# Optimization experiments

Measured on AMD Instinct MI355X. Metric: run time of the kernel, lower is better.

The kernel has to match this reference:

```python
import jax, jax.numpy as jnp
import numpy as np

F_FACETS = 400000
TEX_PER = 4            # textures per facet (counts sum must equal total textures)
T_TEX = F_FACETS * TEX_PER
C_IN = 64
C_OUT = 64
L = 2
N_BASIS = (L + 1) ** 2  # 9
BN_EPS = 1e-3


def setup_inputs() -> dict:
    key = jax.random.key(0)
    k1, k2, k3 = jax.random.split(key, 3)
    input_texture = jax.random.normal(k1, (T_TEX, C_IN), jnp.float32)
    bary_coeff = jax.random.uniform(k2, (T_TEX, N_BASIS), jnp.float32)
    # per-facet texture counts; constant 4 so counts sum exactly to T_TEX
    num_texture = jnp.full((F_FACETS,), TEX_PER, dtype=jnp.int32)
    # xavier_normal_ on [O, I, K]: fan_in = I*K, fan_out = ... torch uses fan_in=I*K? For 3D it treats dim1*rest.
    std = float(np.sqrt(2.0 / (C_IN * N_BASIS + C_OUT * N_BASIS)))
    weights = jax.random.normal(k3, (C_OUT, C_IN, N_BASIS), jnp.float32) * std
    biases = jnp.zeros((1, C_OUT), jnp.float32)
    gamma = jnp.ones((C_OUT,), jnp.float32)
    beta = jnp.zeros((C_OUT,), jnp.float32)
    return {
        "input_texture": input_texture,
        "bary_coeff": bary_coeff,
        "weights": weights,
        "biases": biases,
        "gamma": gamma,
        "beta": beta,
        "num_texture": num_texture,
    }


def reference(input_texture, bary_coeff, weights, biases, gamma, beta, num_texture):
    T = input_texture.shape[0]
    n_facets = num_texture.shape[0]
    n_basis = weights.shape[2]
    # per-texture contribution: contrib[t,o] = sum_{i,k} x[t,i] * W[o,i,k] * bary[t,k]
    # loop over small fixed basis count (9) to avoid a [T, I, K] intermediate
    contrib = jnp.zeros((T, weights.shape[0]), dtype=input_texture.dtype)
    for k in range(n_basis):
        contrib = contrib + (input_texture @ weights[:, :, k].T) * bary_coeff[:, k:k + 1]
    # scatter-sum per facet (ragged groups given by num_texture), then average
    seg_ids = jnp.repeat(jnp.arange(n_facets), num_texture, total_repeat_length=T)
    facet_sum = jax.ops.segment_sum(contrib, seg_ids, num_segments=n_facets)
    out = facet_sum / num_texture[:, None].astype(facet_sum.dtype)
    # bias + ReLU
    out = jax.nn.relu(out + biases)
    # BatchNorm1d in training mode: batch stats (biased variance), eps=1e-3
    mu = jnp.mean(out, axis=0)
    var = jnp.mean(jnp.square(out - mu), axis=0)
    out = (out - mu) * jax.lax.rsqrt(var + BN_EPS) * gamma + beta
    return out
```

## Files before the change

kernel.cpp:

```cpp
#include <hip/hip_runtime.h>


typedef _Float16 half8  __attribute__((ext_vector_type(8)));
typedef _Float16 h2     __attribute__((ext_vector_type(2)));
typedef __fp16   fp16x2 __attribute__((ext_vector_type(2)));
typedef float    f32x4  __attribute__((ext_vector_type(4)));

#define NGROUPS 100000
#define FFACETS 400000
#define GRID1   768
#define LDSBUF  8192

#define WAITV(N) asm volatile("s_waitcnt vmcnt(" #N ")" ::: "memory")
#define FENCE()  asm volatile("" ::: "memory")

union HF { h2 h[4]; half8 v; };

static __device__ __forceinline__ h2 pkrtz(float a, float b) {
    fp16x2 r = __builtin_amdgcn_cvt_pkrtz(a, b);
    return __builtin_bit_cast(h2, r);
}

static __device__ __forceinline__ void gload16(const void* g, void* l) {
    __builtin_amdgcn_global_load_lds((const __attribute__((address_space(1))) void*)g,
                                     (__attribute__((address_space(3))) void*)l, 16, 0, 0);
}

__global__ __launch_bounds__(256) void prep_kernel(const float* __restrict__ W,
                                                   _Float16* __restrict__ wswz,
                                                   float* __restrict__ stats) {
    int idx = blockIdx.x * 256 + threadIdx.x;
    if (idx < 36864) {
        int j    = idx & 7;
        int lane = (idx >> 3) & 63;
        int mt   = (idx >> 9) & 3;
        int c    = idx >> 11;
        int o    = mt * 16 + (lane & 15);
        int i    = (c & 1) * 32 + ((lane >> 4) << 3) + j;
        int kb   = c >> 1;
        wswz[idx] = (_Float16)W[(o * 64 + i) * 9 + kb];
    }
    if (idx < 128) stats[idx] = 0.0f;
}

__global__ __launch_bounds__(256, 3) void pass1_kernel(
    const float* __restrict__ X, const float* __restrict__ BARY,
    const _Float16* __restrict__ WSWZ, const float* __restrict__ BIAS,
    const int* __restrict__ NTEX, float* __restrict__ OUT,
    float* __restrict__ stats) {

    __shared__ __align__(16) char lds[2][LDSBUF];
    __shared__ float sl_s[64];
    __shared__ float sl_s2[64];

    const int tid  = threadIdx.x;
    const int wave = tid >> 6;
    const int lane = tid & 63;
    const int col  = lane & 15;
    const int quad = lane >> 4;

    half8 wf[18];
#pragma unroll
    for (int c = 0; c < 18; ++c)
        wf[c] = *(const half8*)(WSWZ + ((size_t)(c * 4 + wave) * 64 + lane) * 8);

    const f32x4 biasv = *(const f32x4*)(BIAS + wave * 16 + quad * 4);

    const int pphys  = (wave << 10) + (lane << 4);
    const int xsoff  = pphys ^ (((pphys >> 8) & 7) << 4);
    const char* Xb   = (const char*)X;
    const char* BNb  = (lane < 36) ? ((const char*)BARY + lane * 16) : (const char*)NTEX;

    const int m    = (col & 7) << 4;
    const int a00  = (col << 8) + ((quad << 5) ^ m);
    const int a10  = (col << 8) + (((quad << 5) | 16) ^ m);
    const int bco  = 4096 + col * 36;
    const int nco  = 4096 + 576 + ((col >> 2) << 2);

    float sacc[4]  = {0.f, 0.f, 0.f, 0.f};
    float s2acc[4] = {0.f, 0.f, 0.f, 0.f};

    const int b = blockIdx.x;
    const int n = (NGROUPS - 1 - b) / GRID1 + 1;

    auto STAGE = [&](int p, int g) {
        gload16(Xb + (size_t)g * 4096 + xsoff, &lds[p][pphys]);
        if (lane < 37) {
            size_t so = (lane < 36) ? (size_t)g * 576 : (size_t)g * 16;
            gload16(BNb + so, &lds[p][4096 + lane * 16]);
        }
    };

    auto ITER = [&](int p, int g, int gpre, bool do_stage) {
        __builtin_amdgcn_s_barrier();
        FENCE();
        f32x4 r00 = *(const f32x4*)&lds[p][a00];
        f32x4 r10 = *(const f32x4*)&lds[p][a10];
        f32x4 r01 = *(const f32x4*)&lds[p][a00 + 128];
        f32x4 r11 = *(const f32x4*)&lds[p][a10 + 128];
        float bF[9];
#pragma unroll
        for (int k = 0; k < 9; ++k) bF[k] = *(const float*)&lds[p][bco + k * 4];
        const int nt = *(const int*)&lds[p][nco];
        asm volatile("s_waitcnt lgkmcnt(0)" ::: "memory");
        __builtin_amdgcn_sched_barrier(0);
        __builtin_amdgcn_s_barrier();
        FENCE();
        if (do_stage) STAGE(p, gpre);
        FENCE();

        h2 xh[8], bh[9];
        xh[0] = pkrtz(r00[0], r00[1]);  xh[1] = pkrtz(r00[2], r00[3]);
        xh[2] = pkrtz(r10[0], r10[1]);  xh[3] = pkrtz(r10[2], r10[3]);
        xh[4] = pkrtz(r01[0], r01[1]);  xh[5] = pkrtz(r01[2], r01[3]);
        xh[6] = pkrtz(r11[0], r11[1]);  xh[7] = pkrtz(r11[2], r11[3]);
#pragma unroll
        for (int k = 0; k < 9; ++k) bh[k] = pkrtz(bF[k], bF[k]);
        const float rc = __builtin_amdgcn_rcpf((float)nt);

        f32x4 acc0 = {0.f, 0.f, 0.f, 0.f};
        f32x4 acc1 = {0.f, 0.f, 0.f, 0.f};
        __builtin_amdgcn_s_setprio(1);
#pragma unroll
        for (int c = 0; c < 18; c += 2) {
            const h2 bk = bh[c >> 1];
            HF bf0, bf1;
            bf0.h[0] = xh[0] * bk;  bf0.h[1] = xh[1] * bk;
            bf0.h[2] = xh[2] * bk;  bf0.h[3] = xh[3] * bk;
            acc0 = __builtin_amdgcn_mfma_f32_16x16x32_f16(wf[c], bf0.v, acc0, 0, 0, 0);
            bf1.h[0] = xh[4] * bk;  bf1.h[1] = xh[5] * bk;
            bf1.h[2] = xh[6] * bk;  bf1.h[3] = xh[7] * bk;
            acc1 = __builtin_amdgcn_mfma_f32_16x16x32_f16(wf[c + 1], bf1.v, acc1, 0, 0, 0);
        }
        __builtin_amdgcn_s_setprio(0);

        const int f = g * 4 + (col >> 2);
        f32x4 vv;
#pragma unroll
        for (int r = 0; r < 4; ++r) {
            float s = acc0[r] + acc1[r];
            s += __shfl_xor(s, 1);
            s += __shfl_xor(s, 2);
            s = s * rc + biasv[r];
            s = s > 0.f ? s : 0.f;
            vv[r] = s;
            sacc[r]  += s;
            s2acc[r] += s * s;
        }
        if ((col & 3) == 0)
            *(f32x4*)(OUT + (size_t)f * 64 + wave * 16 + quad * 4) = vv;
    };

    STAGE(0, b);
    STAGE(1, b + GRID1);
    WAITV(2); ITER(0, b,         b + 2 * GRID1, true);
    WAITV(3); ITER(1, b + GRID1, b + 3 * GRID1, true);
    int t = 2;
    for (; t < n - 2; ++t) {
        WAITV(4);
        ITER(t & 1, b + t * GRID1, b + (t + 2) * GRID1, true);
    }
    WAITV(4); ITER(t & 1, b + t * GRID1, 0, false); ++t;
    WAITV(0); ITER(t & 1, b + t * GRID1, 0, false);

#pragma unroll
    for (int r = 0; r < 4; ++r) {
        float s = sacc[r], s2 = s2acc[r];
        s  += __shfl_xor(s, 1);  s  += __shfl_xor(s, 2);
        s  += __shfl_xor(s, 4);  s  += __shfl_xor(s, 8);
        s2 += __shfl_xor(s2, 1); s2 += __shfl_xor(s2, 2);
        s2 += __shfl_xor(s2, 4); s2 += __shfl_xor(s2, 8);
        if (col == 0) {
            sl_s [wave * 16 + quad * 4 + r] = s  * 0.25f;
            sl_s2[wave * 16 + quad * 4 + r] = s2 * 0.25f;
        }
    }
    __syncthreads();
    if (tid < 64)        atomicAdd(&stats[tid],      sl_s [tid]);
    else if (tid < 128)  atomicAdd(&stats[tid],      sl_s2[tid - 64]);
}

__global__ __launch_bounds__(256) void pass3_kernel(float* __restrict__ OUT,
    const float* __restrict__ stats, const float* __restrict__ gamma,
    const float* __restrict__ beta) {
    const int tid = threadIdx.x;
    const size_t l = (size_t)blockIdx.x * 256 + tid;
    const int c0 = ((int)l & 15) * 4;
    float mu[4], sc[4], be[4];
    const float invF = 1.0f / (float)FFACETS;
#pragma unroll
    for (int u = 0; u < 4; ++u) {
        int ch = c0 + u;
        float m  = stats[ch] * invF;
        float va = stats[64 + ch] * invF - m * m;
        mu[u] = m;
        sc[u] = rsqrtf(va + 1e-3f) * gamma[ch];
        be[u] = beta[ch];
    }
    const size_t n4 = (size_t)FFACETS * 16;
    for (size_t i = l; i < n4; i += (size_t)gridDim.x * 256) {
        f32x4 v = ((f32x4*)OUT)[i];
#pragma unroll
        for (int u = 0; u < 4; ++u)
            v[u] = (v[u] - mu[u]) * sc[u] + be[u];
        ((f32x4*)OUT)[i] = v;
    }
}

extern "C" void kernel_launch(void* const* d_in, const int* in_sizes, int n_in,
                              void* d_out, int out_size, void* d_ws, size_t ws_size,
                              hipStream_t stream) {
    const float* X     = (const float*)d_in[0];
    const float* BARY  = (const float*)d_in[1];
    const float* W     = (const float*)d_in[2];
    const float* BIAS  = (const float*)d_in[3];
    const float* GAMMA = (const float*)d_in[4];
    const float* BETA  = (const float*)d_in[5];
    const int*   NTEX  = (const int*)d_in[6];
    float* OUT = (float*)d_out;

    _Float16* wswz = (_Float16*)d_ws;
    float* stats   = (float*)((char*)d_ws + 73728);

    prep_kernel<<<144, 256, 0, stream>>>(W, wswz, stats);
    pass1_kernel<<<GRID1, 256, 0, stream>>>(X, BARY, wswz, BIAS, NTEX, OUT, stats);
    pass3_kernel<<<2048, 256, 0, stream>>>(OUT, stats, GAMMA, BETA);
}
```

Measured before the change: 687.9 us.

## Process two facet groups per pipeline iteration with doubled LDS stage

Each pipeline stage now loads two consecutive 16-texture groups (X, barycentric coefficients and counts for 8 facets) into a larger LDS buffer. Each iteration runs two independent 18-MFMA accumulation chains, one per group, instead of splitting one group across two accumulators. The goals are to halve the barrier and stage overhead per group, keep more memory traffic in flight, and give the MFMA units two independent dependency chains to interleave. In exchange the kernel uses more registers and LDS, which may lower occupancy, and the vmcnt wait counts had to be retuned to the new number of loads and stores per stage.

```diff
diff --git a/kernel.cpp b/kernel.cpp
--- a/kernel.cpp
+++ b/kernel.cpp
@@ -7,12 +7,15 @@
 typedef float    f32x4  __attribute__((ext_vector_type(4)));
 
 #define NGROUPS 100000
+#define NPAIRS  50000
 #define FFACETS 400000
 #define GRID1   768
-#define LDSBUF  8192
+#define LDSP    9472
 
 #define WAITV(N) asm volatile("s_waitcnt vmcnt(" #N ")" ::: "memory")
+#define WAITL0() asm volatile("s_waitcnt lgkmcnt(0)" ::: "memory")
 #define FENCE()  asm volatile("" ::: "memory")
+#define SB0()    __builtin_amdgcn_sched_barrier(0)
 
 union HF { h2 h[4]; half8 v; };
 
@@ -49,7 +52,7 @@
     const int* __restrict__ NTEX, float* __restrict__ OUT,
     float* __restrict__ stats) {
 
-    __shared__ __align__(16) char lds[2][LDSBUF];
+    __shared__ __align__(16) char lds[2][LDSP];
     __shared__ float sl_s[64];
     __shared__ float sl_s2[64];
 
@@ -69,76 +72,35 @@
     const int pphys  = (wave << 10) + (lane << 4);
     const int xsoff  = pphys ^ (((pphys >> 8) & 7) << 4);
     const char* Xb   = (const char*)X;
-    const char* BNb  = (lane < 36) ? ((const char*)BARY + lane * 16) : (const char*)NTEX;
+    const char* BAb  = (const char*)BARY;
+    const char* NTb  = (const char*)NTEX;
 
     const int m    = (col & 7) << 4;
     const int a00  = (col << 8) + ((quad << 5) ^ m);
     const int a10  = (col << 8) + (((quad << 5) | 16) ^ m);
-    const int bco  = 4096 + col * 36;
-    const int nco  = 4096 + 576 + ((col >> 2) << 2);
+    const int bco  = 8192 + col * 36;
+    const int nco  = 9344 + ((col >> 2) << 2);
 
     float sacc[4]  = {0.f, 0.f, 0.f, 0.f};
     float s2acc[4] = {0.f, 0.f, 0.f, 0.f};
 
     const int b = blockIdx.x;
-    const int n = (NGROUPS - 1 - b) / GRID1 + 1;
-
-    auto STAGE = [&](int p, int g) {
-        gload16(Xb + (size_t)g * 4096 + xsoff, &lds[p][pphys]);
-        if (lane < 37) {
-            size_t so = (lane < 36) ? (size_t)g * 576 : (size_t)g * 16;
-            gload16(BNb + so, &lds[p][4096 + lane * 16]);
-        }
+    const int n = (NPAIRS - 1 - b) / GRID1 + 1;
+
+    auto STAGE = [&](int p, int u) {
+        const char* xs = Xb + (size_t)u * 8192;
+        gload16(xs + xsoff,        &lds[p][pphys]);
+        gload16(xs + 4096 + xsoff, &lds[p][4096 + pphys]);
+        gload16(BAb + (size_t)u * 1152 + lane * 16, &lds[p][8192 + lane * 16]);
+        if (lane < 8) gload16(BAb + (size_t)u * 1152 + 1024 + lane * 16, &lds[p][9216 + lane * 16]);
+        if (lane < 2) gload16(NTb + (size_t)u * 32 + lane * 16,          &lds[p][9344 + lane * 16]);
     };
 
-    auto ITER = [&](int p, int g, int gpre, bool do_stage) {
-        __builtin_amdgcn_s_barrier();
-        FENCE();
-        f32x4 r00 = *(const f32x4*)&lds[p][a00];
-        f32x4 r10 = *(const f32x4*)&lds[p][a10];
-        f32x4 r01 = *(const f32x4*)&lds[p][a00 + 128];
-        f32x4 r11 = *(const f32x4*)&lds[p][a10 + 128];
-        float bF[9];
-#pragma unroll
-        for (int k = 0; k < 9; ++k) bF[k] = *(const float*)&lds[p][bco + k * 4];
-        const int nt = *(const int*)&lds[p][nco];
-        asm volatile("s_waitcnt lgkmcnt(0)" ::: "memory");
-        __builtin_amdgcn_sched_barrier(0);
-        __builtin_amdgcn_s_barrier();
-        FENCE();
-        if (do_stage) STAGE(p, gpre);
-        FENCE();
-
-        h2 xh[8], bh[9];
-        xh[0] = pkrtz(r00[0], r00[1]);  xh[1] = pkrtz(r00[2], r00[3]);
-        xh[2] = pkrtz(r10[0], r10[1]);  xh[3] = pkrtz(r10[2], r10[3]);
-        xh[4] = pkrtz(r01[0], r01[1]);  xh[5] = pkrtz(r01[2], r01[3]);
-        xh[6] = pkrtz(r11[0], r11[1]);  xh[7] = pkrtz(r11[2], r11[3]);
-#pragma unroll
-        for (int k = 0; k < 9; ++k) bh[k] = pkrtz(bF[k], bF[k]);
-        const float rc = __builtin_amdgcn_rcpf((float)nt);
-
-        f32x4 acc0 = {0.f, 0.f, 0.f, 0.f};
-        f32x4 acc1 = {0.f, 0.f, 0.f, 0.f};
-        __builtin_amdgcn_s_setprio(1);
-#pragma unroll
-        for (int c = 0; c < 18; c += 2) {
-            const h2 bk = bh[c >> 1];
-            HF bf0, bf1;
-            bf0.h[0] = xh[0] * bk;  bf0.h[1] = xh[1] * bk;
-            bf0.h[2] = xh[2] * bk;  bf0.h[3] = xh[3] * bk;
-            acc0 = __builtin_amdgcn_mfma_f32_16x16x32_f16(wf[c], bf0.v, acc0, 0, 0, 0);
-            bf1.h[0] = xh[4] * bk;  bf1.h[1] = xh[5] * bk;
-            bf1.h[2] = xh[6] * bk;  bf1.h[3] = xh[7] * bk;
-            acc1 = __builtin_amdgcn_mfma_f32_16x16x32_f16(wf[c + 1], bf1.v, acc1, 0, 0, 0);
-        }
-        __builtin_amdgcn_s_setprio(0);
-
-        const int f = g * 4 + (col >> 2);
+    auto EPI = [&](f32x4 acc, float rc, int f) {
         f32x4 vv;
 #pragma unroll
         for (int r = 0; r < 4; ++r) {
-            float s = acc0[r] + acc1[r];
+            float s = acc[r];
             s += __shfl_xor(s, 1);
             s += __shfl_xor(s, 2);
             s = s * rc + biasv[r];
@@ -151,17 +113,82 @@
             *(f32x4*)(OUT + (size_t)f * 64 + wave * 16 + quad * 4) = vv;
     };
 
+    auto ITER = [&](int p, int u, int upre, bool do_stage) {
+        __builtin_amdgcn_s_barrier();
+        FENCE();
+        const char* L = lds[p];
+        f32x4 r0[4], r1[4];
+        r0[0] = *(const f32x4*)(L + a00);
+        r0[1] = *(const f32x4*)(L + a10);
+        r0[2] = *(const f32x4*)(L + a00 + 128);
+        r0[3] = *(const f32x4*)(L + a10 + 128);
+        r1[0] = *(const f32x4*)(L + 4096 + a00);
+        r1[1] = *(const f32x4*)(L + 4096 + a10);
+        r1[2] = *(const f32x4*)(L + 4096 + a00 + 128);
+        r1[3] = *(const f32x4*)(L + 4096 + a10 + 128);
+        float bF0[9], bF1[9];
+#pragma unroll
+        for (int k = 0; k < 9; ++k) bF0[k] = *(const float*)(L + bco + k * 4);
+#pragma unroll
+        for (int k = 0; k < 9; ++k) bF1[k] = *(const float*)(L + bco + 576 + k * 4);
+        const int nt0 = *(const int*)(L + nco);
+        const int nt1 = *(const int*)(L + nco + 16);
+
+        h2 xh0[8], xh1[8], bh0[9], bh1[9];
+        xh0[0] = pkrtz(r0[0][0], r0[0][1]);  xh0[1] = pkrtz(r0[0][2], r0[0][3]);
+        xh0[2] = pkrtz(r0[1][0], r0[1][1]);  xh0[3] = pkrtz(r0[1][2], r0[1][3]);
+        xh0[4] = pkrtz(r0[2][0], r0[2][1]);  xh0[5] = pkrtz(r0[2][2], r0[2][3]);
+        xh0[6] = pkrtz(r0[3][0], r0[3][1]);  xh0[7] = pkrtz(r0[3][2], r0[3][3]);
+        xh1[0] = pkrtz(r1[0][0], r1[0][1]);  xh1[1] = pkrtz(r1[0][2], r1[0][3]);
+        xh1[2] = pkrtz(r1[1][0], r1[1][1]);  xh1[3] = pkrtz(r1[1][2], r1[1][3]);
+        xh1[4] = pkrtz(r1[2][0], r1[2][1]);  xh1[5] = pkrtz(r1[2][2], r1[2][3]);
+        xh1[6] = pkrtz(r1[3][0], r1[3][1]);  xh1[7] = pkrtz(r1[3][2], r1[3][3]);
+#pragma unroll
+        for (int k = 0; k < 9; ++k) { bh0[k] = pkrtz(bF0[k], bF0[k]); bh1[k] = pkrtz(bF1[k], bF1[k]); }
+        const float rc0 = __builtin_amdgcn_rcpf((float)nt0);
+        const float rc1 = __builtin_amdgcn_rcpf((float)nt1);
+
+        WAITL0();
+        SB0();
+        __builtin_amdgcn_s_barrier();
+        FENCE();
+        if (do_stage) STAGE(p, upre);
+        FENCE();
+
+        f32x4 accA = {0.f, 0.f, 0.f, 0.f};
+        f32x4 accB = {0.f, 0.f, 0.f, 0.f};
+        __builtin_amdgcn_s_setprio(1);
+#pragma unroll
+        for (int c = 0; c < 18; ++c) {
+            const int hh = (c & 1) * 4;
+            const h2 bkA = bh0[c >> 1];
+            const h2 bkB = bh1[c >> 1];
+            HF fa, fb;
+            fa.h[0] = xh0[hh + 0] * bkA;  fa.h[1] = xh0[hh + 1] * bkA;
+            fa.h[2] = xh0[hh + 2] * bkA;  fa.h[3] = xh0[hh + 3] * bkA;
+            accA = __builtin_amdgcn_mfma_f32_16x16x32_f16(wf[c], fa.v, accA, 0, 0, 0);
+            fb.h[0] = xh1[hh + 0] * bkB;  fb.h[1] = xh1[hh + 1] * bkB;
+            fb.h[2] = xh1[hh + 2] * bkB;  fb.h[3] = xh1[hh + 3] * bkB;
+            accB = __builtin_amdgcn_mfma_f32_16x16x32_f16(wf[c], fb.v, accB, 0, 0, 0);
+        }
+        __builtin_amdgcn_s_setprio(0);
+
+        const int f0 = u * 8 + (col >> 2);
+        EPI(accA, rc0, f0);
+        EPI(accB, rc1, f0 + 4);
+    };
+
     STAGE(0, b);
     STAGE(1, b + GRID1);
-    WAITV(2); ITER(0, b,         b + 2 * GRID1, true);
-    WAITV(3); ITER(1, b + GRID1, b + 3 * GRID1, true);
+    WAITV(5); ITER(0, b,         b + 2 * GRID1, true);
+    WAITV(7); ITER(1, b + GRID1, b + 3 * GRID1, true);
     int t = 2;
     for (; t < n - 2; ++t) {
-        WAITV(4);
+        WAITV(9);
         ITER(t & 1, b + t * GRID1, b + (t + 2) * GRID1, true);
     }
-    WAITV(4); ITER(t & 1, b + t * GRID1, 0, false); ++t;
-    WAITV(0); ITER(t & 1, b + t * GRID1, 0, false);
+    WAITV(9); ITER(t & 1, b + t * GRID1, 0, false); ++t;
+    WAITV(4); ITER(t & 1, b + t * GRID1, 0, false);
 
 #pragma unroll
     for (int r = 0; r < 4; ++r) {
```

Result: faster. 674.4 us (-2.0%).

## Give each wave a private LDS double buffer to drop block barriers

Applied to the files above, without the earlier changes.

Replaces the block-shared double-buffered LDS staging with per-wave private double buffers. Each wave now stages the full X tile, bary coefficients and counts for its group. The two s_barriers per iteration go away and the vmcnt wait counts are adjusted to match. In exchange, every block reads each tile four times from global/L2 and uses more LDS, which may pressure L2 bandwidth and occupancy.

```diff
diff --git a/kernel.cpp b/kernel.cpp
--- a/kernel.cpp
+++ b/kernel.cpp
@@ -9,12 +9,14 @@
 #define NGROUPS 100000
 #define FFACETS 400000
 #define GRID1   768
-#define LDSBUF  8192
+#define LDSW    4688
 
 #define WAITV(N) asm volatile("s_waitcnt vmcnt(" #N ")" ::: "memory")
+#define WAITL0() asm volatile("s_waitcnt lgkmcnt(0)" ::: "memory")
 #define FENCE()  asm volatile("" ::: "memory")
-
-union HF { h2 h[4]; half8 v; };
+#define SB0()    __builtin_amdgcn_sched_barrier(0)
+
+union H8 { h2 h[4]; half8 v; };
 
 static __device__ __forceinline__ h2 pkrtz(float a, float b) {
     fp16x2 r = __builtin_amdgcn_cvt_pkrtz(a, b);
@@ -49,7 +51,7 @@
     const int* __restrict__ NTEX, float* __restrict__ OUT,
     float* __restrict__ stats) {
 
-    __shared__ __align__(16) char lds[2][LDSBUF];
+    __shared__ __align__(16) char ldsbuf[8 * LDSW];
     __shared__ float sl_s[64];
     __shared__ float sl_s2[64];
 
@@ -65,17 +67,24 @@
         wf[c] = *(const half8*)(WSWZ + ((size_t)(c * 4 + wave) * 64 + lane) * 8);
 
     const f32x4 biasv = *(const f32x4*)(BIAS + wave * 16 + quad * 4);
-
-    const int pphys  = (wave << 10) + (lane << 4);
-    const int xsoff  = pphys ^ (((pphys >> 8) & 7) << 4);
-    const char* Xb   = (const char*)X;
-    const char* BNb  = (lane < 36) ? ((const char*)BARY + lane * 16) : (const char*)NTEX;
-
-    const int m    = (col & 7) << 4;
-    const int a00  = (col << 8) + ((quad << 5) ^ m);
-    const int a10  = (col << 8) + (((quad << 5) | 16) ^ m);
-    const int bco  = 4096 + col * 36;
-    const int nco  = 4096 + 576 + ((col >> 2) << 2);
+    FENCE(); SB0();
+
+    int xsoff[4];
+#pragma unroll
+    for (int j = 0; j < 4; ++j)
+        xsoff[j] = (j << 10) + ((lane << 4) ^ ((((j << 2) + (lane >> 4)) & 7) << 4));
+    const char* Xb  = (const char*)X;
+    const char* BAb = (const char*)BARY;
+    const char* NTb = (const char*)NTEX;
+
+    int xrd[4];
+#pragma unroll
+    for (int j = 0; j < 4; ++j) {
+        const int g = (quad << 5) + ((j & 1) << 4) + ((j >> 1) << 7);
+        xrd[j] = (col << 8) + (g ^ ((col & 7) << 4));
+    }
+    const int bco = 4096 + col * 36;
+    const int nco = 4096 + 576 + ((col >> 2) << 2);
 
     float sacc[4]  = {0.f, 0.f, 0.f, 0.f};
     float s2acc[4] = {0.f, 0.f, 0.f, 0.f};
@@ -83,62 +92,29 @@
     const int b = blockIdx.x;
     const int n = (NGROUPS - 1 - b) / GRID1 + 1;
 
-    auto STAGE = [&](int p, int g) {
-        gload16(Xb + (size_t)g * 4096 + xsoff, &lds[p][pphys]);
+    char* B0 = ldsbuf + wave * (2 * LDSW);
+    char* B1 = B0 + LDSW;
+
+    auto STAGE = [&](char* S, int u) {
+        const char* xs = Xb + (size_t)u * 4096;
+        FENCE();
+        gload16(xs + xsoff[0], S);
+        gload16(xs + xsoff[1], S + 1024);
+        gload16(xs + xsoff[2], S + 2048);
+        gload16(xs + xsoff[3], S + 3072);
         if (lane < 37) {
-            size_t so = (lane < 36) ? (size_t)g * 576 : (size_t)g * 16;
-            gload16(BNb + so, &lds[p][4096 + lane * 16]);
-        }
+            const char* g = (lane < 36) ? (BAb + (size_t)u * 576 + lane * 16)
+                                        : (NTb + (size_t)u * 16);
+            gload16(g, S + 4096 + lane * 16);
+        }
+        FENCE();
     };
 
-    auto ITER = [&](int p, int g, int gpre, bool do_stage) {
-        __builtin_amdgcn_s_barrier();
-        FENCE();
-        f32x4 r00 = *(const f32x4*)&lds[p][a00];
-        f32x4 r10 = *(const f32x4*)&lds[p][a10];
-        f32x4 r01 = *(const f32x4*)&lds[p][a00 + 128];
-        f32x4 r11 = *(const f32x4*)&lds[p][a10 + 128];
-        float bF[9];
-#pragma unroll
-        for (int k = 0; k < 9; ++k) bF[k] = *(const float*)&lds[p][bco + k * 4];
-        const int nt = *(const int*)&lds[p][nco];
-        asm volatile("s_waitcnt lgkmcnt(0)" ::: "memory");
-        __builtin_amdgcn_sched_barrier(0);
-        __builtin_amdgcn_s_barrier();
-        FENCE();
-        if (do_stage) STAGE(p, gpre);
-        FENCE();
-
-        h2 xh[8], bh[9];
-        xh[0] = pkrtz(r00[0], r00[1]);  xh[1] = pkrtz(r00[2], r00[3]);
-        xh[2] = pkrtz(r10[0], r10[1]);  xh[3] = pkrtz(r10[2], r10[3]);
-        xh[4] = pkrtz(r01[0], r01[1]);  xh[5] = pkrtz(r01[2], r01[3]);
-        xh[6] = pkrtz(r11[0], r11[1]);  xh[7] = pkrtz(r11[2], r11[3]);
-#pragma unroll
-        for (int k = 0; k < 9; ++k) bh[k] = pkrtz(bF[k], bF[k]);
-        const float rc = __builtin_amdgcn_rcpf((float)nt);
-
-        f32x4 acc0 = {0.f, 0.f, 0.f, 0.f};
-        f32x4 acc1 = {0.f, 0.f, 0.f, 0.f};
-        __builtin_amdgcn_s_setprio(1);
-#pragma unroll
-        for (int c = 0; c < 18; c += 2) {
-            const h2 bk = bh[c >> 1];
-            HF bf0, bf1;
-            bf0.h[0] = xh[0] * bk;  bf0.h[1] = xh[1] * bk;
-            bf0.h[2] = xh[2] * bk;  bf0.h[3] = xh[3] * bk;
-            acc0 = __builtin_amdgcn_mfma_f32_16x16x32_f16(wf[c], bf0.v, acc0, 0, 0, 0);
-            bf1.h[0] = xh[4] * bk;  bf1.h[1] = xh[5] * bk;
-            bf1.h[2] = xh[6] * bk;  bf1.h[3] = xh[7] * bk;
-            acc1 = __builtin_amdgcn_mfma_f32_16x16x32_f16(wf[c + 1], bf1.v, acc1, 0, 0, 0);
-        }
-        __builtin_amdgcn_s_setprio(0);
-
-        const int f = g * 4 + (col >> 2);
+    auto EPI = [&](f32x4 acc, float rc, int f) {
         f32x4 vv;
 #pragma unroll
         for (int r = 0; r < 4; ++r) {
-            float s = acc0[r] + acc1[r];
+            float s = acc[r];
             s += __shfl_xor(s, 1);
             s += __shfl_xor(s, 2);
             s = s * rc + biasv[r];
@@ -151,17 +127,67 @@
             *(f32x4*)(OUT + (size_t)f * 64 + wave * 16 + quad * 4) = vv;
     };
 
-    STAGE(0, b);
-    STAGE(1, b + GRID1);
-    WAITV(2); ITER(0, b,         b + 2 * GRID1, true);
-    WAITV(3); ITER(1, b + GRID1, b + 3 * GRID1, true);
+    auto ITER = [&](char* L, int u, int upre, bool do_stage) {
+        f32x4 r[4];
+#pragma unroll
+        for (int j = 0; j < 4; ++j) r[j] = *(const f32x4*)(L + xrd[j]);
+        float bF[9];
+#pragma unroll
+        for (int k = 0; k < 9; ++k) bF[k] = *(const float*)(L + bco + k * 4);
+        const int nt = *(const int*)(L + nco);
+
+        H8 xlo, xhi;
+        xlo.h[0] = pkrtz(r[0][0], r[0][1]);  xlo.h[1] = pkrtz(r[0][2], r[0][3]);
+        xlo.h[2] = pkrtz(r[1][0], r[1][1]);  xlo.h[3] = pkrtz(r[1][2], r[1][3]);
+        xhi.h[0] = pkrtz(r[2][0], r[2][1]);  xhi.h[1] = pkrtz(r[2][2], r[2][3]);
+        xhi.h[2] = pkrtz(r[3][0], r[3][1]);  xhi.h[3] = pkrtz(r[3][2], r[3][3]);
+        h2 bh[9];
+#pragma unroll
+        for (int k = 0; k < 9; ++k) bh[k] = pkrtz(bF[k], bF[k]);
+        const float rc = __builtin_amdgcn_rcpf((float)nt);
+
+        WAITL0();
+        SB0();
+        if (do_stage) STAGE(L, upre);
+        FENCE();
+
+        f32x4 acc0, acc1;
+        __builtin_amdgcn_s_setprio(1);
+#pragma unroll
+        for (int c = 0; c < 18; ++c) {
+            const h2 bk = bh[c >> 1];
+            H8 bf;
+            if (c & 1) {
+                bf.h[0] = xhi.h[0] * bk;  bf.h[1] = xhi.h[1] * bk;
+                bf.h[2] = xhi.h[2] * bk;  bf.h[3] = xhi.h[3] * bk;
+            } else {
+                bf.h[0] = xlo.h[0] * bk;  bf.h[1] = xlo.h[1] * bk;
+                bf.h[2] = xlo.h[2] * bk;  bf.h[3] = xlo.h[3] * bk;
+            }
+            if (c == 0)      acc0 = __builtin_amdgcn_mfma_f32_16x16x32_f16(wf[c], bf.v, (f32x4){0,0,0,0}, 0, 0, 0);
+            else if (c == 1) acc1 = __builtin_amdgcn_mfma_f32_16x16x32_f16(wf[c], bf.v, (f32x4){0,0,0,0}, 0, 0, 0);
+            else if (c & 1)  acc1 = __builtin_amdgcn_mfma_f32_16x16x32_f16(wf[c], bf.v, acc1, 0, 0, 0);
+            else             acc0 = __builtin_amdgcn_mfma_f32_16x16x32_f16(wf[c], bf.v, acc0, 0, 0, 0);
+        }
+        __builtin_amdgcn_s_setprio(0);
+        f32x4 acc;
+#pragma unroll
+        for (int r = 0; r < 4; ++r) acc[r] = acc0[r] + acc1[r];
+
+        EPI(acc, rc, u * 4 + (col >> 2));
+    };
+
+    STAGE(B0, b);
+    STAGE(B1, b + GRID1);
+    WAITV(5); ITER(B0, b,         b + 2 * GRID1, true);
+    WAITV(6); ITER(B1, b + GRID1, b + 3 * GRID1, true);
     int t = 2;
     for (; t < n - 2; ++t) {
-        WAITV(4);
-        ITER(t & 1, b + t * GRID1, b + (t + 2) * GRID1, true);
-    }
-    WAITV(4); ITER(t & 1, b + t * GRID1, 0, false); ++t;
-    WAITV(0); ITER(t & 1, b + t * GRID1, 0, false);
+        WAITV(7);
+        ITER((t & 1) ? B1 : B0, b + t * GRID1, b + (t + 2) * GRID1, true);
+    }
+    WAITV(7); ITER((t & 1) ? B1 : B0, b + t * GRID1, 0, false); ++t;
+    WAITV(2); ITER((t & 1) ? B1 : B0, b + t * GRID1, 0, false);
 
 #pragma unroll
     for (int r = 0; r < 4; ++r) {
```

Result: slower. 701.7 us (+2.0%).
